# Kernel optimization log

Hardware: AMD Instinct MI355X
Metric: run time of the kernel (lower is better)

Reference implementation:

```python
import jax, jax.numpy as jnp
import numpy as np

D_MODEL = 1024
N_HEAD = 16
D_K = D_MODEL // N_HEAD


def setup_inputs() -> dict:
    key = jax.random.key(0)
    ks = jax.random.split(key, 11)
    B, S, D = 2, 2048, D_MODEL
    scale = 1.0 / np.sqrt(D)
    inp = {
        "q": jax.random.normal(ks[0], (B, S, D), jnp.float32),
        "k": jax.random.normal(ks[1], (B, S, D), jnp.float32),
        "v": jax.random.normal(ks[2], (B, S, D), jnp.float32),
        "w_q": jax.random.normal(ks[3], (D, D), jnp.float32) * scale,
        "b_q": jnp.zeros((D,), jnp.float32),
        "w_k": jax.random.normal(ks[4], (D, D), jnp.float32) * scale,
        "b_k": jnp.zeros((D,), jnp.float32),
        "w_v": jax.random.normal(ks[5], (D, D), jnp.float32) * scale,
        "b_v": jnp.zeros((D,), jnp.float32),
        "w_o": jax.random.normal(ks[6], (D, D), jnp.float32) * scale,
        "b_o": jnp.zeros((D,), jnp.float32),
    }
    return inp


def _split_heads(x):
    # torch: chunk(n_head, dim=-1) then cat(dim=0) -> [H*B, S, d_k]
    B, S, D = x.shape
    x = x.reshape(B, S, N_HEAD, D_K)            # contiguous last-dim chunks
    return x.transpose(2, 0, 1, 3).reshape(N_HEAD * B, S, D_K)


def _merge_heads(x, B):
    # torch: chunk(n_head, dim=0) then cat(dim=-1) -> [B, S, D]
    HB, S, dk = x.shape
    x = x.reshape(N_HEAD, B, S, dk).transpose(1, 2, 0, 3)
    return x.reshape(B, S, N_HEAD * dk)


def reference(q, k, v, w_q, b_q, w_k, b_k, w_v, b_v, w_o, b_o):
    B = q.shape[0]
    qh = _split_heads(q @ w_q + b_q)            # [H*B, S, d_k]
    kh = _split_heads(k @ w_k + b_k)
    vh = _split_heads(v @ w_v + b_v)
    # scaled dot-product attention (naive, materializes scores)
    scores = jnp.einsum('bqd,bkd->bqk', qh, kh) / jnp.sqrt(jnp.float32(D_K))
    attn = jax.nn.softmax(scores, axis=-1)
    out = jnp.einsum('bqk,bkd->bqd', attn, vh)  # [H*B, S, d_k]
    out = _merge_heads(out, B)                  # [B, S, D]
    return out @ w_o + b_o
```

## Files before the change

kernel.cpp:

```cpp
#include <hip/hip_runtime.h>
#include <hip/hip_bf16.h>
#include <stdint.h>

#define DEVINL __device__ __forceinline__

typedef __attribute__((ext_vector_type(8))) short bf16x8;
typedef __attribute__((ext_vector_type(4))) short short4v;
typedef __attribute__((ext_vector_type(8))) unsigned short ushort8;
typedef __attribute__((ext_vector_type(4))) float f32x4;
typedef __attribute__((ext_vector_type(16))) float f32x16;
typedef __attribute__((ext_vector_type(4))) int int4v;

DEVINL unsigned short f2bf(float x) {
  union { float f; uint32_t u; } v; v.f = x;
  uint32_t u = v.u;
  u += 0x7fffu + ((u >> 16) & 1u);
  return (unsigned short)(u >> 16);
}

DEVINL int pack_bf16x2(float lo, float hi) {
  __hip_bfloat162 bb = __float22bfloat162_rn(make_float2(lo, hi));
  int r;
  __builtin_memcpy(&r, &bb, 4);
  return r;
}

DEVINL void gload_lds16(const void* g, void* l) {
  __builtin_amdgcn_global_load_lds((const __attribute__((address_space(1))) void*)g,
                                   (__attribute__((address_space(3))) void*)l, 16, 0, 0);
}

#define E2(x) __builtin_amdgcn_exp2f(x)

DEVINL void barrier_raw() {
  asm volatile("" ::: "memory");
  __builtin_amdgcn_s_barrier();
  asm volatile("" ::: "memory");
}
#define WAITVM(N) asm volatile("s_waitcnt vmcnt(" #N ")" ::: "memory")

__global__ __launch_bounds__(256) void prep(
    const float* __restrict__ q,  unsigned short* __restrict__ Xq,
    const float* __restrict__ k,  unsigned short* __restrict__ Xk,
    const float* __restrict__ v,  unsigned short* __restrict__ Xv,
    const float* __restrict__ w0, unsigned short* __restrict__ o0,
    const float* __restrict__ w1, unsigned short* __restrict__ o1,
    const float* __restrict__ w2, unsigned short* __restrict__ o2,
    const float* __restrict__ w3, unsigned short* __restrict__ o3) {
  __shared__ float tile[64][65];
  int bid = blockIdx.x;
  int t = threadIdx.x;
  if (bid < 6144) {
    int which = bid >> 11;
    int i = (((bid & 2047) << 8) + t) * 8;
    const float* in = which == 0 ? q : which == 1 ? k : v;
    unsigned short* out = which == 0 ? Xq : which == 1 ? Xk : Xv;
    float4 a = *(const float4*)(in + i);
    float4 b = *(const float4*)(in + i + 4);
    ushort8 r;
    r[0] = f2bf(a.x); r[1] = f2bf(a.y); r[2] = f2bf(a.z); r[3] = f2bf(a.w);
    r[4] = f2bf(b.x); r[5] = f2bf(b.y); r[6] = f2bf(b.z); r[7] = f2bf(b.w);
    *(ushort8*)(out + i) = r;
    return;
  }
  int tb = bid - 6144;
  int z = tb >> 8;
  const float* w = z == 0 ? w0 : z == 1 ? w1 : z == 2 ? w2 : w3;
  unsigned short* wt = z == 0 ? o0 : z == 1 ? o1 : z == 2 ? o2 : o3;
  int n0 = ((tb >> 4) & 15) * 64, k0 = (tb & 15) * 64;
  for (int i = 0; i < 4; ++i) {
    int r = (t >> 4) + i * 16;
    int c = (t & 15) * 4;
    float4 vv = *(const float4*)(w + (size_t)(k0 + r) * 1024 + n0 + c);
    tile[r][c] = vv.x; tile[r][c + 1] = vv.y; tile[r][c + 2] = vv.z; tile[r][c + 3] = vv.w;
  }
  __syncthreads();
  for (int i = 0; i < 4; ++i) {
    int rn = (t >> 4) + i * 16;
    int ck = (t & 15) * 4;
    short4v o;
    o[0] = (short)f2bf(tile[ck + 0][rn]);
    o[1] = (short)f2bf(tile[ck + 1][rn]);
    o[2] = (short)f2bf(tile[ck + 2][rn]);
    o[3] = (short)f2bf(tile[ck + 3][rn]);
    *(short4v*)(wt + (size_t)(n0 + rn) * 1024 + k0 + ck) = o;
  }
}

DEVINL void gemm_body(const unsigned short* __restrict__ A,
                      const unsigned short* __restrict__ Bt,
                      const float* __restrict__ bias,
                      void* __restrict__ out, float scale, int mode,
                      int bx, int by) {
  constexpr int K = 1024;
  __shared__ unsigned short Alds[2 * 128 * 32];
  __shared__ unsigned short Blds[2 * 64 * 32];
  int tile_m = bx * 128;
  int tile_n = by * 64;
  int t = threadIdx.x, lane = t & 63, wid = t >> 6;
  int wm = wid >> 1, wn = wid & 1;
  int fr = lane & 15, fq = lane >> 4;
  f32x4 acc[4][2] = {};

  int ga0 = wid * 64 + lane, ga1 = ga0 + 256;
  int gb0 = wid * 64 + lane;
  int ra0 = ga0 >> 2, ca0 = ((ga0 & 3) ^ ((ra0 >> 1) & 3)) * 8;
  int ra1 = ga1 >> 2, ca1 = ((ga1 & 3) ^ ((ra1 >> 1) & 3)) * 8;
  int rb0 = gb0 >> 2, cb0 = ((gb0 & 3) ^ ((rb0 >> 1) & 3)) * 8;
  const unsigned short* Abase = A  + (size_t)tile_m * K;
  const unsigned short* Bbase = Bt + (size_t)tile_n * K;

  int aoff[4], boff[2];
#pragma unroll
  for (int i = 0; i < 4; ++i) {
    int r = wm * 64 + i * 16 + fr;
    aoff[i] = (r * 4 + (fq ^ ((r >> 1) & 3))) * 8;
  }
#pragma unroll
  for (int j = 0; j < 2; ++j) {
    int r = wn * 32 + j * 16 + fr;
    boff[j] = (r * 4 + (fq ^ ((r >> 1) & 3))) * 8;
  }

  auto stage = [&](int nb, int k0) {
    gload_lds16(Abase + (size_t)ra0 * K + k0 + ca0, Alds + nb * 4096 + ga0 * 8);
    gload_lds16(Abase + (size_t)ra1 * K + k0 + ca1, Alds + nb * 4096 + ga1 * 8);
    gload_lds16(Bbase + (size_t)rb0 * K + k0 + cb0, Blds + nb * 2048 + gb0 * 8);
  };
  auto compute = [&](int nb) {
    bf16x8 af[4], bfb[2];
#pragma unroll
    for (int i = 0; i < 4; ++i) af[i] = *(const bf16x8*)(Alds + nb * 4096 + aoff[i]);
#pragma unroll
    for (int j = 0; j < 2; ++j) bfb[j] = *(const bf16x8*)(Blds + nb * 2048 + boff[j]);
#pragma unroll
    for (int i = 0; i < 4; ++i)
#pragma unroll
      for (int j = 0; j < 2; ++j)
        acc[i][j] = __builtin_amdgcn_mfma_f32_16x16x32_bf16(af[i], bfb[j], acc[i][j], 0, 0, 0);
  };

  stage(0, 0);
  stage(1, 32);
  WAITVM(3);
  barrier_raw();
  for (int it = 0; it < 15; ++it) {
    compute(0);
    barrier_raw();
    stage(0, 64 * it + 64);
    WAITVM(3);
    barrier_raw();
    compute(1);
    barrier_raw();
    stage(1, 64 * it + 96);
    WAITVM(3);
    barrier_raw();
  }
  compute(0);
  barrier_raw();
  WAITVM(0);
  barrier_raw();
  compute(1);

  int fqs = ((fq & 1) << 1) | (fq >> 1);
#pragma unroll
  for (int i = 0; i < 4; ++i) {
#pragma unroll
    for (int j = 0; j < 2; ++j) {
      int n = tile_n + wn * 32 + j * 16 + fr;
      float bv = bias[n];
      int m0 = tile_m + wm * 64 + i * 16 + fq * 4;
      if (mode == 0) {
        size_t base = (size_t)((n >> 6) * 2 + (m0 >> 11)) * (2048 * 64) + (n & 63);
#pragma unroll
        for (int r = 0; r < 4; ++r)
          ((unsigned short*)out)[base + (size_t)((m0 + r) & 2047) * 64] =
              f2bf((acc[i][j][r] + bv) * scale);
      } else if (mode == 2) {
        int m0s = tile_m + wm * 64 + i * 16 + fqs * 4;
        size_t base = (size_t)((n >> 6) * 2 + (m0 >> 11)) * (64 * 2048)
                    + (size_t)(n & 63) * 2048 + (m0s & 2047);
        short4v o;
#pragma unroll
        for (int r = 0; r < 4; ++r) o[r] = (short)f2bf(acc[i][j][r] + bv);
        *(short4v*)((unsigned short*)out + base) = o;
      } else {
#pragma unroll
        for (int r = 0; r < 4; ++r)
          ((float*)out)[(size_t)(m0 + r) * 1024 + n] = acc[i][j][r] + bv;
      }
    }
  }
}

__global__ __launch_bounds__(256) void gemm_qkv(
    const unsigned short* __restrict__ Xq, const unsigned short* __restrict__ Xk,
    const unsigned short* __restrict__ Xv,
    const unsigned short* __restrict__ Wtq, const unsigned short* __restrict__ Wtk,
    const unsigned short* __restrict__ Wtv,
    const float* __restrict__ bq, const float* __restrict__ bk,
    const float* __restrict__ bv,
    unsigned short* __restrict__ Qh, unsigned short* __restrict__ Kh,
    unsigned short* __restrict__ Vt, float qscale) {
  int z = blockIdx.z;
  const unsigned short* A  = z == 0 ? Xq : z == 1 ? Xk : Xv;
  const unsigned short* Bt = z == 0 ? Wtq : z == 1 ? Wtk : Wtv;
  const float* bias        = z == 0 ? bq : z == 1 ? bk : bv;
  void* out                = z == 0 ? (void*)Qh : z == 1 ? (void*)Kh : (void*)Vt;
  float scale = z == 0 ? qscale : 1.0f;
  int mode = z == 2 ? 2 : 0;
  gemm_body(A, Bt, bias, out, scale, mode, blockIdx.x, blockIdx.y);
}

__global__ __launch_bounds__(256) void gemm_o(
    const unsigned short* __restrict__ A, const unsigned short* __restrict__ Bt,
    const float* __restrict__ bias, float* __restrict__ out) {
  gemm_body(A, Bt, bias, out, 1.0f, 1, blockIdx.x, blockIdx.y);
}

__global__ __launch_bounds__(256) void attn_fwd(
    const unsigned short* __restrict__ Qh,
    const unsigned short* __restrict__ Kh,
    const unsigned short* __restrict__ Vtg,
    unsigned short* __restrict__ O) {
  constexpr int S = 2048, DK = 64;
  __shared__ unsigned short Klds[2 * 64 * 64];
  __shared__ unsigned short Vlds[2 * 64 * 64];

  int wg = blockIdx.x;
  int swz = (wg & 7) * 64 + (wg >> 3);
  int hb = swz >> 4;
  int qt = swz & 15;
  int t = threadIdx.x, lane = t & 63, wid = t >> 6;
  int lq = lane & 31, hi = lane >> 5;
  int q0 = qt * 128;

  const unsigned short* Qb = Qh  + (size_t)hb * S * DK;
  const unsigned short* Kb = Kh  + (size_t)hb * S * DK;
  const unsigned short* Vb = Vtg + (size_t)hb * DK * S;

  bf16x8 qf[4];
#pragma unroll
  for (int kk = 0; kk < 4; ++kk)
    qf[kk] = *(const bf16x8*)(Qb + (size_t)(q0 + wid * 32 + lq) * DK + kk * 16 + hi * 8);

  int g0 = wid * 128 + lane, g1 = g0 + 64;
  int sr0 = g0 >> 3, sc0 = ((g0 & 7) ^ (sr0 & 7)) * 8;
  int sr1 = g1 >> 3, sc1 = ((g1 & 7) ^ (sr1 & 7)) * 8;

  int koff[2][4], voff[2][4];
#pragma unroll
  for (int h2 = 0; h2 < 2; ++h2) {
    int row = 32 * h2 + lq;
#pragma unroll
    for (int kk = 0; kk < 4; ++kk)
      koff[h2][kk] = (row * 8 + ((2 * kk + hi) ^ (row & 7))) * 8;
  }
#pragma unroll
  for (int jt = 0; jt < 2; ++jt) {
    int row = 32 * jt + lq;
#pragma unroll
    for (int ks = 0; ks < 4; ++ks)
      voff[jt][ks] = (row * 8 + ((2 * ks + hi) ^ (row & 7))) * 8;
  }

  auto stage = [&](int nb, int kt) {
    const unsigned short* Ksrc = Kb + (size_t)kt * 64 * DK;
    const unsigned short* Vsrc = Vb + (size_t)kt * 64;
    gload_lds16(Ksrc + sr0 * 64 + sc0, Klds + nb * 4096 + g0 * 8);
    gload_lds16(Ksrc + sr1 * 64 + sc1, Klds + nb * 4096 + g1 * 8);
    gload_lds16(Vsrc + (size_t)sr0 * S + sc0, Vlds + nb * 4096 + g0 * 8);
    gload_lds16(Vsrc + (size_t)sr1 * S + sc1, Vlds + nb * 4096 + g1 * 8);
  };

  float m = -INFINITY;
  float ps4[4] = {0.f, 0.f, 0.f, 0.f};
  f32x16 oacc[2] = {};

  auto tilestep = [&](int nb) {
    const unsigned short* Kc = Klds + nb * 4096;
    const unsigned short* Vc = Vlds + nb * 4096;

    f32x16 sacc[2] = {};
    __builtin_amdgcn_s_setprio(1);
#pragma unroll
    for (int kk = 0; kk < 4; ++kk) {
      bf16x8 k0 = *(const bf16x8*)(Kc + koff[0][kk]);
      sacc[0] = __builtin_amdgcn_mfma_f32_32x32x16_bf16(k0, qf[kk], sacc[0], 0, 0, 0);
      bf16x8 k1 = *(const bf16x8*)(Kc + koff[1][kk]);
      sacc[1] = __builtin_amdgcn_mfma_f32_32x32x16_bf16(k1, qf[kk], sacc[1], 0, 0, 0);
    }
    __builtin_amdgcn_s_setprio(0);

    float pmax = fmaxf(sacc[0][0], sacc[0][1]);
#pragma unroll
    for (int r = 2; r < 16; r += 2) pmax = fmaxf(pmax, fmaxf(sacc[0][r], sacc[0][r + 1]));
#pragma unroll
    for (int r = 0; r < 16; r += 2) pmax = fmaxf(pmax, fmaxf(sacc[1][r], sacc[1][r + 1]));
    pmax = fmaxf(pmax, __shfl_xor(pmax, 32, 64));

    if (!__all(pmax <= m + 8.0f)) {
      float mn = fmaxf(m, pmax);
      float cf = E2(m - mn);
      m = mn;
#pragma unroll
      for (int bnk = 0; bnk < 4; ++bnk) ps4[bnk] *= cf;
#pragma unroll
      for (int jt = 0; jt < 2; ++jt)
#pragma unroll
        for (int r = 0; r < 16; ++r) oacc[jt][r] *= cf;
    }

#pragma unroll
    for (int r = 0; r < 16; ++r) {
      float p0 = E2(sacc[0][r] - m);
      float p1 = E2(sacc[1][r] - m);
      sacc[0][r] = p0; sacc[1][r] = p1;
      ps4[r & 3] += p0 + p1;
    }

    bf16x8 pfrag[4];
#pragma unroll
    for (int ks = 0; ks < 4; ++ks) {
      const int h2 = ks >> 1, b = 8 * (ks & 1);
      int4v w;
      w[0] = pack_bf16x2(sacc[h2][b + 0], sacc[h2][b + 1]);
      w[1] = pack_bf16x2(sacc[h2][b + 2], sacc[h2][b + 3]);
      w[2] = pack_bf16x2(sacc[h2][b + 4], sacc[h2][b + 5]);
      w[3] = pack_bf16x2(sacc[h2][b + 6], sacc[h2][b + 7]);
      pfrag[ks] = __builtin_bit_cast(bf16x8, w);
    }

    __builtin_amdgcn_s_setprio(1);
#pragma unroll
    for (int jt = 0; jt < 2; ++jt)
#pragma unroll
      for (int ks = 0; ks < 4; ++ks) {
        bf16x8 vf = *(const bf16x8*)(Vc + voff[jt][ks]);
        oacc[jt] = __builtin_amdgcn_mfma_f32_32x32x16_bf16(vf, pfrag[ks], oacc[jt], 0, 0, 0);
      }
    __builtin_amdgcn_s_setprio(0);
  };

  stage(0, 0);
  __syncthreads();
  for (int it = 0; it < 16; ++it) {
    int t1 = 2 * it + 1, t2 = 2 * it + 2;
    stage(1, t1);
    tilestep(0);
    __syncthreads();
    if (t2 < 32) stage(0, t2);
    tilestep(1);
    __syncthreads();
  }

  float l = (ps4[0] + ps4[1]) + (ps4[2] + ps4[3]);
  l += __shfl_xor(l, 32, 64);

  int h = hb >> 1, b = hb & 1;
  int q = q0 + wid * 32 + lq;
  float linv = 1.0f / l;
  unsigned short* orow = O + (size_t)(b * 2048 + q) * 1024 + h * 64;
#pragma unroll
  for (int jt = 0; jt < 2; ++jt)
#pragma unroll
    for (int g = 0; g < 4; ++g) {
      short4v o;
#pragma unroll
      for (int r = 0; r < 4; ++r) o[r] = (short)f2bf(oacc[jt][4 * g + r] * linv);
      *(short4v*)(orow + jt * 32 + 8 * g + 4 * hi) = o;
    }
}

extern "C" void kernel_launch(void* const* d_in, const int* in_sizes, int n_in,
                              void* d_out, int out_size, void* d_ws, size_t ws_size,
                              hipStream_t stream) {
  const float* q   = (const float*)d_in[0];
  const float* k   = (const float*)d_in[1];
  const float* v   = (const float*)d_in[2];
  const float* w_q = (const float*)d_in[3];
  const float* b_q = (const float*)d_in[4];
  const float* w_k = (const float*)d_in[5];
  const float* b_k = (const float*)d_in[6];
  const float* w_v = (const float*)d_in[7];
  const float* b_v = (const float*)d_in[8];
  const float* w_o = (const float*)d_in[9];
  const float* b_o = (const float*)d_in[10];

  char* ws = (char*)d_ws;
  unsigned short* Xq  = (unsigned short*)(ws + 0);
  unsigned short* Xk  = (unsigned short*)(ws + 8388608);
  unsigned short* Xv  = (unsigned short*)(ws + 16777216);
  unsigned short* Wtq = (unsigned short*)(ws + 25165824);
  unsigned short* Wtk = (unsigned short*)(ws + 27262976);
  unsigned short* Wtv = (unsigned short*)(ws + 29360128);
  unsigned short* Wto = (unsigned short*)(ws + 31457280);
  unsigned short* Qh  = (unsigned short*)(ws + 33554432);
  unsigned short* Kh  = (unsigned short*)(ws + 41943040);
  unsigned short* Vt  = (unsigned short*)(ws + 50331648);
  unsigned short* Obuf = Xq;

  prep<<<7168, 256, 0, stream>>>(q, Xq, k, Xk, v, Xv,
                                 w_q, Wtq, w_k, Wtk, w_v, Wtv, w_o, Wto);

  const float qscale = 0.125f * 1.44269504088896340736f;
  dim3 gq(32, 16, 3);
  gemm_qkv<<<gq, 256, 0, stream>>>(Xq, Xk, Xv, Wtq, Wtk, Wtv,
                                   b_q, b_k, b_v, Qh, Kh, Vt, qscale);

  attn_fwd<<<512, 256, 0, stream>>>(Qh, Kh, Vt, Obuf);

  dim3 gg(32, 16);
  gemm_o<<<gg, 256, 0, stream>>>(Obuf, Wto, b_o, (float*)d_out);
}
```

Before: 141.4 us.

## Process 128-key tiles per attention step to halve barriers and softmax rescale checks

The attention kernel now stages two 64-key K/V sub-tiles per buffer, 128 keys per step, and runs the online-softmax max/rescale once per 128 keys instead of per 64. This halves the number of __syncthreads and rescale branches and gives more MFMA work between barriers. In exchange, LDS use doubles to 64KB, which may reduce occupancy, and more accumulator registers are held live.

```diff
diff --git a/kernel.cpp b/kernel.cpp
--- a/kernel.cpp
+++ b/kernel.cpp
@@ -224,8 +224,8 @@
     const unsigned short* __restrict__ Vtg,
     unsigned short* __restrict__ O) {
   constexpr int S = 2048, DK = 64;
-  __shared__ unsigned short Klds[2 * 64 * 64];
-  __shared__ unsigned short Vlds[2 * 64 * 64];
+  __shared__ unsigned short Klds[2 * 2 * 64 * 64];
+  __shared__ unsigned short Vlds[2 * 2 * 64 * 64];
 
   int wg = blockIdx.x;
   int swz = (wg & 7) * 64 + (wg >> 3);
@@ -264,39 +264,49 @@
       voff[jt][ks] = (row * 8 + ((2 * ks + hi) ^ (row & 7))) * 8;
   }
 
-  auto stage = [&](int nb, int kt) {
-    const unsigned short* Ksrc = Kb + (size_t)kt * 64 * DK;
-    const unsigned short* Vsrc = Vb + (size_t)kt * 64;
-    gload_lds16(Ksrc + sr0 * 64 + sc0, Klds + nb * 4096 + g0 * 8);
-    gload_lds16(Ksrc + sr1 * 64 + sc1, Klds + nb * 4096 + g1 * 8);
-    gload_lds16(Vsrc + (size_t)sr0 * S + sc0, Vlds + nb * 4096 + g0 * 8);
-    gload_lds16(Vsrc + (size_t)sr1 * S + sc1, Vlds + nb * 4096 + g1 * 8);
+  auto stage = [&](int nb, int bt) {
+#pragma unroll
+    for (int sub = 0; sub < 2; ++sub) {
+      int kt = 2 * bt + sub;
+      const unsigned short* Ksrc = Kb + (size_t)kt * 64 * DK;
+      const unsigned short* Vsrc = Vb + (size_t)kt * 64;
+      unsigned short* Kd = Klds + nb * 8192 + sub * 4096;
+      unsigned short* Vd = Vlds + nb * 8192 + sub * 4096;
+      gload_lds16(Ksrc + sr0 * 64 + sc0, Kd + g0 * 8);
+      gload_lds16(Ksrc + sr1 * 64 + sc1, Kd + g1 * 8);
+      gload_lds16(Vsrc + (size_t)sr0 * S + sc0, Vd + g0 * 8);
+      gload_lds16(Vsrc + (size_t)sr1 * S + sc1, Vd + g1 * 8);
+    }
   };
 
   float m = -INFINITY;
   float ps4[4] = {0.f, 0.f, 0.f, 0.f};
   f32x16 oacc[2] = {};
 
-  auto tilestep = [&](int nb) {
-    const unsigned short* Kc = Klds + nb * 4096;
-    const unsigned short* Vc = Vlds + nb * 4096;
-
-    f32x16 sacc[2] = {};
+  auto bigstep = [&](int nb) {
+    const unsigned short* Kc = Klds + nb * 8192;
+    const unsigned short* Vc = Vlds + nb * 8192;
+
+    f32x16 sacc[4] = {};
     __builtin_amdgcn_s_setprio(1);
 #pragma unroll
     for (int kk = 0; kk < 4; ++kk) {
-      bf16x8 k0 = *(const bf16x8*)(Kc + koff[0][kk]);
-      sacc[0] = __builtin_amdgcn_mfma_f32_32x32x16_bf16(k0, qf[kk], sacc[0], 0, 0, 0);
-      bf16x8 k1 = *(const bf16x8*)(Kc + koff[1][kk]);
-      sacc[1] = __builtin_amdgcn_mfma_f32_32x32x16_bf16(k1, qf[kk], sacc[1], 0, 0, 0);
+#pragma unroll
+      for (int sub = 0; sub < 2; ++sub) {
+        bf16x8 k0 = *(const bf16x8*)(Kc + sub * 4096 + koff[0][kk]);
+        sacc[2 * sub] = __builtin_amdgcn_mfma_f32_32x32x16_bf16(k0, qf[kk], sacc[2 * sub], 0, 0, 0);
+        bf16x8 k1 = *(const bf16x8*)(Kc + sub * 4096 + koff[1][kk]);
+        sacc[2 * sub + 1] = __builtin_amdgcn_mfma_f32_32x32x16_bf16(k1, qf[kk], sacc[2 * sub + 1], 0, 0, 0);
+      }
     }
     __builtin_amdgcn_s_setprio(0);
 
     float pmax = fmaxf(sacc[0][0], sacc[0][1]);
 #pragma unroll
-    for (int r = 2; r < 16; r += 2) pmax = fmaxf(pmax, fmaxf(sacc[0][r], sacc[0][r + 1]));
-#pragma unroll
-    for (int r = 0; r < 16; r += 2) pmax = fmaxf(pmax, fmaxf(sacc[1][r], sacc[1][r + 1]));
+    for (int s = 0; s < 4; ++s)
+#pragma unroll
+      for (int r = (s == 0 ? 2 : 0); r < 16; r += 2)
+        pmax = fmaxf(pmax, fmaxf(sacc[s][r], sacc[s][r + 1]));
     pmax = fmaxf(pmax, __shfl_xor(pmax, 32, 64));
 
     if (!__all(pmax <= m + 8.0f)) {
@@ -312,45 +322,48 @@
     }
 
 #pragma unroll
-    for (int r = 0; r < 16; ++r) {
-      float p0 = E2(sacc[0][r] - m);
-      float p1 = E2(sacc[1][r] - m);
-      sacc[0][r] = p0; sacc[1][r] = p1;
-      ps4[r & 3] += p0 + p1;
-    }
-
-    bf16x8 pfrag[4];
-#pragma unroll
-    for (int ks = 0; ks < 4; ++ks) {
-      const int h2 = ks >> 1, b = 8 * (ks & 1);
-      int4v w;
-      w[0] = pack_bf16x2(sacc[h2][b + 0], sacc[h2][b + 1]);
-      w[1] = pack_bf16x2(sacc[h2][b + 2], sacc[h2][b + 3]);
-      w[2] = pack_bf16x2(sacc[h2][b + 4], sacc[h2][b + 5]);
-      w[3] = pack_bf16x2(sacc[h2][b + 6], sacc[h2][b + 7]);
-      pfrag[ks] = __builtin_bit_cast(bf16x8, w);
-    }
+    for (int s = 0; s < 4; ++s)
+#pragma unroll
+      for (int r = 0; r < 16; ++r) {
+        float p = E2(sacc[s][r] - m);
+        sacc[s][r] = p;
+        ps4[r & 3] += p;
+      }
 
     __builtin_amdgcn_s_setprio(1);
 #pragma unroll
-    for (int jt = 0; jt < 2; ++jt)
+    for (int sub = 0; sub < 2; ++sub) {
+      bf16x8 pfrag[4];
 #pragma unroll
       for (int ks = 0; ks < 4; ++ks) {
-        bf16x8 vf = *(const bf16x8*)(Vc + voff[jt][ks]);
-        oacc[jt] = __builtin_amdgcn_mfma_f32_32x32x16_bf16(vf, pfrag[ks], oacc[jt], 0, 0, 0);
+        const int s = 2 * sub + (ks >> 1), b = 8 * (ks & 1);
+        int4v w;
+        w[0] = pack_bf16x2(sacc[s][b + 0], sacc[s][b + 1]);
+        w[1] = pack_bf16x2(sacc[s][b + 2], sacc[s][b + 3]);
+        w[2] = pack_bf16x2(sacc[s][b + 4], sacc[s][b + 5]);
+        w[3] = pack_bf16x2(sacc[s][b + 6], sacc[s][b + 7]);
+        pfrag[ks] = __builtin_bit_cast(bf16x8, w);
       }
+#pragma unroll
+      for (int jt = 0; jt < 2; ++jt)
+#pragma unroll
+        for (int ks = 0; ks < 4; ++ks) {
+          bf16x8 vf = *(const bf16x8*)(Vc + sub * 4096 + voff[jt][ks]);
+          oacc[jt] = __builtin_amdgcn_mfma_f32_32x32x16_bf16(vf, pfrag[ks], oacc[jt], 0, 0, 0);
+        }
+    }
     __builtin_amdgcn_s_setprio(0);
   };
 
   stage(0, 0);
   __syncthreads();
-  for (int it = 0; it < 16; ++it) {
+  for (int it = 0; it < 8; ++it) {
     int t1 = 2 * it + 1, t2 = 2 * it + 2;
     stage(1, t1);
-    tilestep(0);
+    bigstep(0);
     __syncthreads();
-    if (t2 < 32) stage(0, t2);
-    tilestep(1);
+    if (t2 < 16) stage(0, t2);
+    bigstep(1);
     __syncthreads();
   }
 
```

Result: slower. 150.4 us (+6.4%).
